# Performance work log

Measured on AMD Instinct MI355X. Metric: run time of the kernel, lower is better.

The kernel has to match this reference:

```python
import jax, jax.numpy as jnp
import numpy as np

D_MODEL = 1024
NUM_HEADS = 16
HEAD_DIM = D_MODEL // NUM_HEADS  # 64
SCALE = HEAD_DIM ** -0.5
BIAS_LEN = 128  # min(max_seq_len=512, 128)
ROPE_BASE = 10000.0
LN_EPS = 1e-5


def setup_inputs() -> dict:
    key = jax.random.key(0)
    ks = jax.random.split(key, 8)
    B, Lq, Lkv = 8, 512, 512
    return {
        "decoder_hidden": jax.random.normal(ks[0], (B, Lq, D_MODEL), jnp.float32),
        "encoder_output": jax.random.normal(ks[1], (B, Lkv, D_MODEL), jnp.float32),
        "Wqkv": jax.random.normal(ks[2], (3 * D_MODEL, D_MODEL), jnp.float32) * 0.02,
        "Wout": jax.random.normal(ks[3], (D_MODEL, D_MODEL), jnp.float32) * 0.02,
        "b_out": jnp.zeros((D_MODEL,), jnp.float32),
        "Wgate": jax.random.normal(ks[4], (D_MODEL, D_MODEL), jnp.float32) * 0.02,
        "b_gate": jnp.zeros((D_MODEL,), jnp.float32),
        "gamma": jnp.ones((D_MODEL,), jnp.float32),
        "beta": jnp.zeros((D_MODEL,), jnp.float32),
    }


def _layernorm(x, gamma, beta):
    mu = jnp.mean(x, axis=-1, keepdims=True)
    var = jnp.mean(jnp.square(x - mu), axis=-1, keepdims=True)
    return (x - mu) * jax.lax.rsqrt(var + LN_EPS) * gamma + beta


def _rope(x, cos, sin):
    # x: [B, H, L, HEAD_DIM]; cos/sin: [L, HEAD_DIM//2]
    half = HEAD_DIM // 2
    c = cos[None, None, :, :]
    s = sin[None, None, :, :]
    x_even, x_odd = x[..., :half], x[..., half:]
    return jnp.concatenate([x_even * c - x_odd * s, x_even * s + x_odd * c], axis=-1)


def _temporal_bias(L_q, L_kv):
    pos = jnp.arange(BIAS_LEN, dtype=jnp.float32)
    dist = jnp.abs(pos[None, :] - pos[:, None])  # [128,128]
    bias = jnp.exp(-dist * 0.1) - dist * 0.05
    if L_q <= BIAS_LEN and L_kv <= BIAS_LEN:
        return bias[:L_q, :L_kv]
    # bilinear interpolation (align_corners=False / half-pixel) fallback
    return jax.image.resize(bias, (L_q, L_kv), method="bilinear")


def reference(decoder_hidden, encoder_output, Wqkv, Wout, b_out, Wgate, b_gate, gamma, beta):
    B, L_q, _ = decoder_hidden.shape
    L_kv = encoder_output.shape[1]
    residual = decoder_hidden

    q_in = _layernorm(decoder_hidden, gamma, beta)
    kv_in = _layernorm(encoder_output, gamma, beta)

    q = q_in @ Wqkv[:D_MODEL].T
    k = kv_in @ Wqkv[D_MODEL:2 * D_MODEL].T
    v = kv_in @ Wqkv[2 * D_MODEL:].T

    q = q.reshape(B, L_q, NUM_HEADS, HEAD_DIM).transpose(0, 2, 1, 3)
    k = k.reshape(B, L_kv, NUM_HEADS, HEAD_DIM).transpose(0, 2, 1, 3)
    v = v.reshape(B, L_kv, NUM_HEADS, HEAD_DIM).transpose(0, 2, 1, 3)

    # rotary embedding over max(L_q, L_kv) positions
    L = max(L_q, L_kv)
    inv_freq = 1.0 / ROPE_BASE ** (jnp.arange(0, HEAD_DIM, 2, dtype=jnp.float32) / HEAD_DIM)
    freqs = jnp.arange(L, dtype=jnp.float32)[:, None] * inv_freq[None, :]  # [L, HEAD_DIM//2]
    cos, sin = jnp.cos(freqs), jnp.sin(freqs)
    q = _rope(q, cos[:L_q], sin[:L_q])
    k = _rope(k, cos[:L_kv], sin[:L_kv])

    scores = jnp.einsum("bhqd,bhkd->bhqk", q, k) * SCALE
    scores = scores + _temporal_bias(L_q, L_kv)[None, None, :, :]

    attn = jax.nn.softmax(scores, axis=-1)
    attended = jnp.einsum("bhqk,bhkd->bhqd", attn, v)
    attended = attended.transpose(0, 2, 1, 3).reshape(B, L_q, D_MODEL)
    attended = attended @ Wout.T + b_out

    gate = jax.nn.sigmoid(attended @ Wgate.T + b_gate)
    output = gate * attended + (1.0 - gate) * residual
    return output
```

## Files before the change

kernel.cpp:

```cpp
#include <hip/hip_runtime.h>
#include <hip/hip_bf16.h>

#define D_MODEL 1024
#define NHEADS 16
#define HDIM 64
#define BATCH 8
#define SEQ 512
#define NROWS 4096
#define SCALE 0.125f
#define LN_EPS 1e-5f

typedef __attribute__((ext_vector_type(8))) short bf16x8;
typedef __attribute__((ext_vector_type(4))) float f32x4;
typedef __attribute__((ext_vector_type(8))) unsigned short u16x8;

static __device__ __forceinline__ float bf2f(unsigned short u) {
    return __uint_as_float(((unsigned int)u) << 16);
}
static __device__ __forceinline__ unsigned short f2bf(float f) {
    unsigned int x = __float_as_uint(f);
    unsigned int r = (x + 0x7fffu + ((x >> 16) & 1u)) >> 16;
    return (unsigned short)r;
}

#define GLOAD16(gp, lp)                                                        \
    __builtin_amdgcn_global_load_lds(                                          \
        (const __attribute__((address_space(1))) void*)(gp),                   \
        (__attribute__((address_space(3))) void*)(lp), 16, 0, 0)

static __device__ __forceinline__ float bias128(int a, int b) {
    float d = fabsf((float)(a - b));
    return expf(-d * 0.1f) - d * 0.05f;
}

__global__ void prep_kernel(const float* __restrict__ dec, const float* __restrict__ enc,
                            const float* __restrict__ gamma, const float* __restrict__ beta,
                            const float* __restrict__ Wqkv,
                            unsigned short* __restrict__ q_ln, unsigned short* __restrict__ kv_ln,
                            float* __restrict__ bias, unsigned short* __restrict__ Wqkv_bf) {
    int blk = blockIdx.x;
    int t = threadIdx.x;
    if (blk >= 9216) {
        int idx = (blk - 9216) * 256 + t;
        float4 v = ((const float4*)Wqkv)[idx];
        ushort4 u;
        u.x = f2bf(v.x); u.y = f2bf(v.y); u.z = f2bf(v.z); u.w = f2bf(v.w);
        ((ushort4*)Wqkv_bf)[idx] = u;
        return;
    }
    if (blk >= 8192) {
        int idx = (blk - 8192) * 256 + t;
        int qi = idx >> 9, kj = idx & 511;
        float fq = (qi + 0.5f) * 0.25f - 0.5f;
        float fk = (kj + 0.5f) * 0.25f - 0.5f;
        int iq = (int)floorf(fq); float tq = fq - (float)iq;
        int ik = (int)floorf(fk); float tk = fk - (float)ik;
        int iq0 = min(max(iq, 0), 127), iq1 = min(max(iq + 1, 0), 127);
        int ik0 = min(max(ik, 0), 127), ik1 = min(max(ik + 1, 0), 127);
        float v = (1.f - tq) * ((1.f - tk) * bias128(iq0, ik0) + tk * bias128(iq0, ik1))
                +        tq  * ((1.f - tk) * bias128(iq1, ik0) + tk * bias128(iq1, ik1));
        bias[idx] = v;
        return;
    }
    int row = blk;
    const float* src = (row < NROWS) ? dec + (size_t)row * D_MODEL
                                     : enc + (size_t)(row - NROWS) * D_MODEL;
    unsigned short* dst = (row < NROWS) ? q_ln + (size_t)row * D_MODEL
                                        : kv_ln + (size_t)(row - NROWS) * D_MODEL;
    float4 x = ((const float4*)src)[t];
    float s  = x.x + x.y + x.z + x.w;
    float ss = x.x * x.x + x.y * x.y + x.z * x.z + x.w * x.w;
    #pragma unroll
    for (int off = 32; off > 0; off >>= 1) {
        s  += __shfl_down(s, off);
        ss += __shfl_down(ss, off);
    }
    __shared__ float red_s[4], red_ss[4];
    int wid = t >> 6, lane = t & 63;
    if (lane == 0) { red_s[wid] = s; red_ss[wid] = ss; }
    __syncthreads();
    if (t == 0) {
        float S = red_s[0] + red_s[1] + red_s[2] + red_s[3];
        float SS = red_ss[0] + red_ss[1] + red_ss[2] + red_ss[3];
        red_s[0] = S; red_ss[0] = SS;
    }
    __syncthreads();
    float mu  = red_s[0] * (1.0f / 1024.0f);
    float var = red_ss[0] * (1.0f / 1024.0f) - mu * mu;
    float rstd = rsqrtf(var + LN_EPS);
    float4 g = ((const float4*)gamma)[t];
    float4 bb = ((const float4*)beta)[t];
    ushort4 u;
    u.x = f2bf((x.x - mu) * rstd * g.x + bb.x);
    u.y = f2bf((x.y - mu) * rstd * g.y + bb.y);
    u.z = f2bf((x.z - mu) * rstd * g.z + bb.z);
    u.w = f2bf((x.w - mu) * rstd * g.w + bb.w);
    ((ushort4*)dst)[t] = u;
}

__global__ void convert_og(const float* __restrict__ Wout, const float* __restrict__ Wgate,
                           unsigned short* __restrict__ Wout_bf, unsigned short* __restrict__ Wgate_bf) {
    int idx = blockIdx.x * 256 + threadIdx.x;
    const float* src; unsigned short* dst; int off;
    if (idx < 262144) { src = (const float*)Wout; dst = Wout_bf; off = idx; }
    else              { src = (const float*)Wgate; dst = Wgate_bf; off = idx - 262144; }
    float4 v = ((const float4*)src)[off];
    ushort4 u;
    u.x = f2bf(v.x); u.y = f2bf(v.y); u.z = f2bf(v.z); u.w = f2bf(v.w);
    ((ushort4*)dst)[off] = u;
}

#define CSTR 136

union alignas(16) GemmSmem {
    struct { unsigned short A[128 * 64]; unsigned short B[128 * 64]; } ab;
    unsigned short C[128 * CSTR];
};

struct alignas(16) Smem64 {
    unsigned short A[64 * 64];
    unsigned short B[128 * 64];
};

#define MF(a, b, d) __builtin_amdgcn_mfma_f32_16x16x32_bf16((a), (b), (d), 0, 0, 0)

#define GEMM_KH(kh)                                                            \
    {                                                                          \
        const unsigned short* Arow_ = &As[(wr * 64 + c) * 64 + pofs##kh];      \
        const unsigned short* Brow_ = &Bs[(wc * 64 + c) * 64 + pofs##kh];      \
        bf16x8 f0 = *(const bf16x8*)(Arow_);                                   \
        bf16x8 f1 = *(const bf16x8*)(Arow_ + 1024);                            \
        bf16x8 f2 = *(const bf16x8*)(Arow_ + 2048);                            \
        bf16x8 f3 = *(const bf16x8*)(Arow_ + 3072);                            \
        bf16x8 g0 = *(const bf16x8*)(Brow_);                                   \
        bf16x8 g1 = *(const bf16x8*)(Brow_ + 1024);                            \
        bf16x8 g2 = *(const bf16x8*)(Brow_ + 2048);                            \
        bf16x8 g3 = *(const bf16x8*)(Brow_ + 3072);                            \
        a00 = MF(f0, g0, a00); a01 = MF(f0, g1, a01); a02 = MF(f0, g2, a02); a03 = MF(f0, g3, a03); \
        a10 = MF(f1, g0, a10); a11 = MF(f1, g1, a11); a12 = MF(f1, g2, a12); a13 = MF(f1, g3, a13); \
        a20 = MF(f2, g0, a20); a21 = MF(f2, g1, a21); a22 = MF(f2, g2, a22); a23 = MF(f2, g3, a23); \
        a30 = MF(f3, g0, a30); a31 = MF(f3, g1, a31); a32 = MF(f3, g2, a32); a33 = MF(f3, g3, a33); \
    }

#define GEMM_MAIN_LOOP(Aptr, Bptr)                                             \
    __shared__ GemmSmem smem;                                                  \
    unsigned short* As = smem.ab.A;                                            \
    unsigned short* Bs = smem.ab.B;                                            \
    int tid = threadIdx.x;                                                     \
    int wave = tid >> 6, lane = tid & 63, quad = lane >> 4, c = lane & 15;     \
    int wr = wave >> 1, wc = wave & 1;                                         \
    int x7 = c & 7;                                                            \
    int pofs0 = (quad ^ x7) * 8;                                               \
    int pofs1 = ((4 + quad) ^ x7) * 8;                                         \
    int grow = lane >> 3;                                                      \
    int cg = ((lane & 7) ^ grow) * 8;                                          \
    const unsigned short* Ag = (Aptr) + (size_t)(rt * 128 + wave * 32 + grow) * 1024 + cg; \
    const unsigned short* Bg = (Bptr) + (size_t)(ct * 128 + wave * 32 + grow) * 1024 + cg; \
    unsigned short* AsW = As + wave * 2048;                                    \
    unsigned short* BsW = Bs + wave * 2048;                                    \
    f32x4 a00 = (f32x4)0.f, a01 = (f32x4)0.f, a02 = (f32x4)0.f, a03 = (f32x4)0.f; \
    f32x4 a10 = (f32x4)0.f, a11 = (f32x4)0.f, a12 = (f32x4)0.f, a13 = (f32x4)0.f; \
    f32x4 a20 = (f32x4)0.f, a21 = (f32x4)0.f, a22 = (f32x4)0.f, a23 = (f32x4)0.f; \
    f32x4 a30 = (f32x4)0.f, a31 = (f32x4)0.f, a32 = (f32x4)0.f, a33 = (f32x4)0.f; \
    for (int kt = 0; kt < 16; ++kt) {                                          \
        int k0 = kt * 64;                                                      \
        __syncthreads();                                                       \
        GLOAD16(Ag + k0,         AsW);                                         \
        GLOAD16(Ag + 8192 + k0,  AsW + 512);                                   \
        GLOAD16(Ag + 16384 + k0, AsW + 1024);                                  \
        GLOAD16(Ag + 24576 + k0, AsW + 1536);                                  \
        GLOAD16(Bg + k0,         BsW);                                         \
        GLOAD16(Bg + 8192 + k0,  BsW + 512);                                   \
        GLOAD16(Bg + 16384 + k0, BsW + 1024);                                  \
        GLOAD16(Bg + 24576 + k0, BsW + 1536);                                  \
        __syncthreads();                                                       \
        GEMM_KH(0)                                                             \
        GEMM_KH(1)                                                             \
    }

#define GEMM_KH2(kh)                                                           \
    {                                                                          \
        const unsigned short* Arow_ = &As2[(wr * 32 + c) * 64 + pofs##kh];     \
        const unsigned short* Brow_ = &Bs2[(wc * 64 + c) * 64 + pofs##kh];     \
        bf16x8 f0 = *(const bf16x8*)(Arow_);                                   \
        bf16x8 f1 = *(const bf16x8*)(Arow_ + 1024);                            \
        bf16x8 g0 = *(const bf16x8*)(Brow_);                                   \
        bf16x8 g1 = *(const bf16x8*)(Brow_ + 1024);                            \
        bf16x8 g2 = *(const bf16x8*)(Brow_ + 2048);                            \
        bf16x8 g3 = *(const bf16x8*)(Brow_ + 3072);                            \
        c00 = MF(f0, g0, c00); c01 = MF(f0, g1, c01); c02 = MF(f0, g2, c02); c03 = MF(f0, g3, c03); \
        c10 = MF(f1, g0, c10); c11 = MF(f1, g1, c11); c12 = MF(f1, g2, c12); c13 = MF(f1, g3, c13); \
    }

#define GEMM_LOOP_64(Aptr, Bptr)                                               \
    __shared__ Smem64 smem2;                                                   \
    unsigned short* As2 = smem2.A;                                             \
    unsigned short* Bs2 = smem2.B;                                             \
    int tid = threadIdx.x;                                                     \
    int wave = tid >> 6, lane = tid & 63, quad = lane >> 4, c = lane & 15;     \
    int wr = wave >> 1, wc = wave & 1;                                         \
    int x7 = c & 7;                                                            \
    int pofs0 = (quad ^ x7) * 8;                                               \
    int pofs1 = ((4 + quad) ^ x7) * 8;                                         \
    int grow = lane >> 3;                                                      \
    int cg = ((lane & 7) ^ grow) * 8;                                          \
    const unsigned short* Ag = (Aptr) + (size_t)(rt * 64 + wave * 16 + grow) * 1024 + cg;  \
    const unsigned short* Bg = (Bptr) + (size_t)(ct * 128 + wave * 32 + grow) * 1024 + cg; \
    unsigned short* AsW = As2 + wave * 1024;                                   \
    unsigned short* BsW = Bs2 + wave * 2048;                                   \
    f32x4 c00 = (f32x4)0.f, c01 = (f32x4)0.f, c02 = (f32x4)0.f, c03 = (f32x4)0.f; \
    f32x4 c10 = (f32x4)0.f, c11 = (f32x4)0.f, c12 = (f32x4)0.f, c13 = (f32x4)0.f; \
    for (int kt = 0; kt < 16; ++kt) {                                          \
        int k0 = kt * 64;                                                      \
        __syncthreads();                                                       \
        GLOAD16(Ag + k0,         AsW);                                         \
        GLOAD16(Ag + 8192 + k0,  AsW + 512);                                   \
        GLOAD16(Bg + k0,         BsW);                                         \
        GLOAD16(Bg + 8192 + k0,  BsW + 512);                                   \
        GLOAD16(Bg + 16384 + k0, BsW + 1024);                                  \
        GLOAD16(Bg + 24576 + k0, BsW + 1536);                                  \
        __syncthreads();                                                       \
        GEMM_KH2(0)                                                            \
        GEMM_KH2(1)                                                            \
    }

#define ROPE_REG(i, reg, A0, A1, A2, A3)                                       \
    {                                                                          \
        int mloc = wr * 64 + (i) * 16 + quad * 4 + (reg);                      \
        int crow = mloc * CSTR + wc * 64;                                      \
        float fl = (float)((rt * 128 + mloc) & 511);                           \
        float aa0 = fl * inv0, aa1 = fl * inv1;                                \
        float c0 = cosf(aa0), s0 = sinf(aa0);                                  \
        float c1 = cosf(aa1), s1 = sinf(aa1);                                  \
        float e0 = A0[(reg)], o0 = A2[(reg)];                                  \
        float e1 = A1[(reg)], o1 = A3[(reg)];                                  \
        smem.C[crow + c]      = f2bf(e0 * c0 - o0 * s0);                       \
        smem.C[crow + 32 + c] = f2bf(e0 * s0 + o0 * c0);                       \
        smem.C[crow + 16 + c] = f2bf(e1 * c1 - o1 * s1);                       \
        smem.C[crow + 48 + c] = f2bf(e1 * s1 + o1 * c1);                       \
    }
#define ROPE_ROW(i, A0, A1, A2, A3)                                            \
    ROPE_REG(i, 0, A0, A1, A2, A3) ROPE_REG(i, 1, A0, A1, A2, A3)              \
    ROPE_REG(i, 2, A0, A1, A2, A3) ROPE_REG(i, 3, A0, A1, A2, A3)

#define VSEC_REG(i, reg, A0, A1, A2, A3)                                       \
    {                                                                          \
        int crow = (wr * 64 + (i) * 16 + quad * 4 + (reg)) * CSTR + wc * 64;   \
        smem.C[crow + c]      = f2bf(A0[(reg)]);                               \
        smem.C[crow + 16 + c] = f2bf(A1[(reg)]);                               \
        smem.C[crow + 32 + c] = f2bf(A2[(reg)]);                               \
        smem.C[crow + 48 + c] = f2bf(A3[(reg)]);                               \
    }
#define VSEC_ROW(i, A0, A1, A2, A3)                                            \
    VSEC_REG(i, 0, A0, A1, A2, A3) VSEC_REG(i, 1, A0, A1, A2, A3)              \
    VSEC_REG(i, 2, A0, A1, A2, A3) VSEC_REG(i, 3, A0, A1, A2, A3)

__global__ __launch_bounds__(256, 1)
void qkv_gemm_mfma(const unsigned short* __restrict__ q_ln,
                   const unsigned short* __restrict__ kv_ln,
                   const unsigned short* __restrict__ Wb,
                   unsigned short* __restrict__ qo,
                   unsigned short* __restrict__ ko,
                   unsigned short* __restrict__ vo) {
    int bid = blockIdx.x;
    int st = bid >> 5, in = bid & 31;
    int stc = st % 3, str = st / 3;
    int ct = stc * 8 + (in & 7);
    int rt = str * 4 + (in >> 3);
    int n0 = ct * 128;
    int section = n0 >> 10;
    const unsigned short* A = (section == 0) ? q_ln : kv_ln;

    GEMM_MAIN_LOOP(A, Wb)

    __syncthreads();
    if (section == 2) {
        VSEC_ROW(0, a00, a01, a02, a03)
        VSEC_ROW(1, a10, a11, a12, a13)
        VSEC_ROW(2, a20, a21, a22, a23)
        VSEC_ROW(3, a30, a31, a32, a33)
    } else {
        float inv0 = expf(-0.2878231366f * (float)c);
        float inv1 = expf(-0.2878231366f * (float)(16 + c));
        ROPE_ROW(0, a00, a01, a02, a03)
        ROPE_ROW(1, a10, a11, a12, a13)
        ROPE_ROW(2, a20, a21, a22, a23)
        ROPE_ROW(3, a30, a31, a32, a33)
    }
    __syncthreads();

    unsigned short* outp = (section == 0) ? qo : (section == 1) ? ko : vo;
    int rr = tid >> 1, ch = tid & 1;
    int mm = rt * 128 + rr;
    int bb = mm >> 9, ll = mm & 511;
    int h = ((n0 & 1023) >> 6) + ch;
    unsigned short* orow = outp + (((size_t)bb * NHEADS + h) * SEQ + ll) * HDIM;
    const unsigned short* csrc = &smem.C[rr * CSTR + ch * 64];
    #pragma unroll
    for (int kc = 0; kc < 8; ++kc)
        *(u16x8*)(orow + kc * 8) = *(const u16x8*)(csrc + kc * 8);
}

#define O1_REG(mb, reg, n, Acc)                                                \
    t_bf[(size_t)((mb) + (reg)) * 1024 + (n)] = f2bf(Acc[(reg)] + bo);
#define O1_TILE(i, j, Acc)                                                     \
    {                                                                          \
        int n = ct * 128 + wc * 64 + (j) * 16 + c;                             \
        float bo = b_out[n];                                                   \
        int mb = rt * 64 + wr * 32 + (i) * 16 + quad * 4;                      \
        O1_REG(mb, 0, n, Acc) O1_REG(mb, 1, n, Acc)                            \
        O1_REG(mb, 2, n, Acc) O1_REG(mb, 3, n, Acc)                            \
    }

__global__ __launch_bounds__(256, 1)
void out_gemm1_mfma(const unsigned short* __restrict__ att,
                    const unsigned short* __restrict__ Wob,
                    const float* __restrict__ b_out,
                    unsigned short* __restrict__ t_bf) {
    int ct = blockIdx.x, rt = blockIdx.y;

    GEMM_LOOP_64(att, Wob)

    O1_TILE(0, 0, c00) O1_TILE(0, 1, c01) O1_TILE(0, 2, c02) O1_TILE(0, 3, c03)
    O1_TILE(1, 0, c10) O1_TILE(1, 1, c11) O1_TILE(1, 2, c12) O1_TILE(1, 3, c13)
}

#define O2_REG(mb, reg, n, Acc)                                                \
    {                                                                          \
        float gz = Acc[(reg)] + bg;                                            \
        float g = 1.0f / (1.0f + expf(-gz));                                   \
        size_t idx = (size_t)((mb) + (reg)) * 1024 + (n);                      \
        float tv = bf2f(t_bf[idx]);                                            \
        float rv = residual[idx];                                              \
        out[idx] = g * tv + (1.0f - g) * rv;                                   \
    }
#define O2_TILE(i, j, Acc)                                                     \
    {                                                                          \
        int n = ct * 128 + wc * 64 + (j) * 16 + c;                             \
        float bg = b_gate[n];                                                  \
        int mb = rt * 64 + wr * 32 + (i) * 16 + quad * 4;                      \
        O2_REG(mb, 0, n, Acc) O2_REG(mb, 1, n, Acc)                            \
        O2_REG(mb, 2, n, Acc) O2_REG(mb, 3, n, Acc)                            \
    }

__global__ __launch_bounds__(256, 1)
void out_gemm2_mfma(const unsigned short* __restrict__ t_bf,
                    const unsigned short* __restrict__ Wgb,
                    const float* __restrict__ b_gate,
                    const float* __restrict__ residual,
                    float* __restrict__ out) {
    int ct = blockIdx.x, rt = blockIdx.y;

    GEMM_LOOP_64(t_bf, Wgb)

    O2_TILE(0, 0, c00) O2_TILE(0, 1, c01) O2_TILE(0, 2, c02) O2_TILE(0, 3, c03)
    O2_TILE(1, 0, c10) O2_TILE(1, 1, c11) O2_TILE(1, 2, c12) O2_TILE(1, 3, c13)
}

#define KSTR 72

__global__ __launch_bounds__(512)
void attn_kernel(const unsigned short* __restrict__ q,
                 const unsigned short* __restrict__ k,
                 const unsigned short* __restrict__ v,
                 const float* __restrict__ bias,
                 unsigned short* __restrict__ attended) {
    int qt = blockIdx.x, h = blockIdx.y, b = blockIdx.z;
    __shared__ unsigned short Ks[64 * KSTR];
    __shared__ unsigned short Vt[64 * KSTR];
    __shared__ unsigned short Ps[128 * KSTR];
    __shared__ float lf[128];

    int tid = threadIdx.x;
    int wave = tid >> 6, lane = tid & 63;
    int quad = lane >> 4, c = lane & 15;
    int wb = wave * 16;
    size_t headbase = (((size_t)b * NHEADS + h) * SEQ) * HDIM;
    int q0 = qt * 128;

    const unsigned short* qrow = q + headbase + (size_t)(q0 + wb + c) * HDIM;
    bf16x8 aq0 = *(const bf16x8*)(qrow + quad * 8);
    bf16x8 aq1 = *(const bf16x8*)(qrow + 32 + quad * 8);

    int sr = tid >> 3, sc0 = (tid & 7) * 8;

    f32x4 oacc[4];
    #pragma unroll
    for (int t = 0; t < 4; ++t) oacc[t] = (f32x4)0.f;
    float lrow[4];
    #pragma unroll
    for (int r = 0; r < 4; ++r) lrow[r] = 0.f;

    for (int kt = 0; kt < 8; ++kt) {
        int kv0 = kt * 64;
        __syncthreads();
        {
            const unsigned short* krow = k + headbase + (size_t)(kv0 + sr) * HDIM + sc0;
            const unsigned short* vrow = v + headbase + (size_t)(kv0 + sr) * HDIM + sc0;
            u16x8 ka = *(const u16x8*)(krow);
            u16x8 va = *(const u16x8*)(vrow);
            *(u16x8*)&Ks[sr * KSTR + sc0] = ka;
            #pragma unroll
            for (int j = 0; j < 8; ++j) Vt[(sc0 + j) * KSTR + sr] = va[j];
        }
        __syncthreads();

        f32x4 sacc[4];
        #pragma unroll
        for (int nt = 0; nt < 4; ++nt) {
            const unsigned short* kbase = &Ks[(nt * 16 + c) * KSTR];
            bf16x8 b0 = *(const bf16x8*)(kbase + quad * 8);
            bf16x8 b1 = *(const bf16x8*)(kbase + 32 + quad * 8);
            f32x4 a = (f32x4)0.f;
            a = __builtin_amdgcn_mfma_f32_16x16x32_bf16(aq0, b0, a, 0, 0, 0);
            a = __builtin_amdgcn_mfma_f32_16x16x32_bf16(aq1, b1, a, 0, 0, 0);
            sacc[nt] = a;
        }

        const float* bbase = bias + (size_t)(q0 + wb + quad * 4) * 512 + kv0 + c;
        float tsum[4];
        #pragma unroll
        for (int r = 0; r < 4; ++r) tsum[r] = 0.f;
        #pragma unroll
        for (int nt = 0; nt < 4; ++nt)
            #pragma unroll
            for (int r = 0; r < 4; ++r) {
                float p = __expf(sacc[nt][r] * SCALE + bbase[(size_t)r * 512 + nt * 16]);
                tsum[r] += p;
                Ps[(wb + quad * 4 + r) * KSTR + nt * 16 + c] = f2bf(p);
            }
        #pragma unroll
        for (int r = 0; r < 4; ++r) {
            float t = tsum[r];
            t += __shfl_xor(t, 1);
            t += __shfl_xor(t, 2);
            t += __shfl_xor(t, 4);
            t += __shfl_xor(t, 8);
            lrow[r] += t;
        }

        bf16x8 pb0 = *(const bf16x8*)&Ps[(wb + c) * KSTR + quad * 8];
        bf16x8 pb1 = *(const bf16x8*)&Ps[(wb + c) * KSTR + 32 + quad * 8];
        #pragma unroll
        for (int t = 0; t < 4; ++t) {
            const unsigned short* vbase = &Vt[(t * 16 + c) * KSTR];
            bf16x8 a0 = *(const bf16x8*)(vbase + quad * 8);
            bf16x8 a1 = *(const bf16x8*)(vbase + 32 + quad * 8);
            oacc[t] = __builtin_amdgcn_mfma_f32_16x16x32_bf16(a0, pb0, oacc[t], 0, 0, 0);
            oacc[t] = __builtin_amdgcn_mfma_f32_16x16x32_bf16(a1, pb1, oacc[t], 0, 0, 0);
        }
    }

    if (c == 0) {
        f32x4 lv;
        lv[0] = lrow[0]; lv[1] = lrow[1]; lv[2] = lrow[2]; lv[3] = lrow[3];
        *(f32x4*)&lf[wb + quad * 4] = lv;
    }
    float invl = 1.0f / lf[wb + c];
    unsigned short* drow = attended + ((size_t)b * SEQ + (q0 + wb + c)) * D_MODEL + h * HDIM;
    #pragma unroll
    for (int t = 0; t < 4; ++t) {
        ushort4 o;
        o.x = f2bf(oacc[t][0] * invl);
        o.y = f2bf(oacc[t][1] * invl);
        o.z = f2bf(oacc[t][2] * invl);
        o.w = f2bf(oacc[t][3] * invl);
        *(ushort4*)(drow + t * 16 + quad * 4) = o;
    }
}

extern "C" void kernel_launch(void* const* d_in, const int* in_sizes, int n_in,
                              void* d_out, int out_size, void* d_ws, size_t ws_size,
                              hipStream_t stream) {
    const float* dec    = (const float*)d_in[0];
    const float* enc    = (const float*)d_in[1];
    const float* Wqkv   = (const float*)d_in[2];
    const float* Wout   = (const float*)d_in[3];
    const float* b_out  = (const float*)d_in[4];
    const float* Wgate  = (const float*)d_in[5];
    const float* b_gate = (const float*)d_in[6];
    const float* gamma  = (const float*)d_in[7];
    const float* beta   = (const float*)d_in[8];
    float* out = (float*)d_out;

    char* ws = (char*)d_ws;
    const size_t MB = 1024 * 1024;
    unsigned short* q_ln    = (unsigned short*)(ws + 0 * MB);
    unsigned short* kv_ln   = (unsigned short*)(ws + 8 * MB);
    unsigned short* qb      = (unsigned short*)(ws + 16 * MB);
    unsigned short* kb      = (unsigned short*)(ws + 24 * MB);
    unsigned short* vb      = (unsigned short*)(ws + 32 * MB);
    unsigned short* Wqkv_bf = (unsigned short*)(ws + 40 * MB);
    float*          bias    = (float*)(ws + 46 * MB);
    unsigned short* att     = (unsigned short*)(ws + 0 * MB);
    unsigned short* t_bf    = (unsigned short*)(ws + 24 * MB);
    unsigned short* Wout_bf = (unsigned short*)(ws + 32 * MB);
    unsigned short* Wgate_bf= (unsigned short*)(ws + 34 * MB);

    prep_kernel<<<12288, 256, 0, stream>>>(dec, enc, gamma, beta, Wqkv,
                                           q_ln, kv_ln, bias, Wqkv_bf);
    qkv_gemm_mfma<<<768, 256, 0, stream>>>(q_ln, kv_ln, Wqkv_bf, qb, kb, vb);
    attn_kernel<<<dim3(4, 16, 8), 512, 0, stream>>>(qb, kb, vb, bias, att);
    convert_og<<<2048, 256, 0, stream>>>(Wout, Wgate, Wout_bf, Wgate_bf);
    out_gemm1_mfma<<<dim3(8, 64), 256, 0, stream>>>(att, Wout_bf, b_out, t_bf);
    out_gemm2_mfma<<<dim3(8, 64), 256, 0, stream>>>(t_bf, Wgate_bf, b_gate, dec, out);
}
```

Baseline: 244.3 us.

## Deepen K tile in output GEMMs and fold Wout/Wgate conversion into prep

The two output-projection GEMMs now stage 128-wide K slices instead of 64, halving the loop trip count and the number of barrier pairs per K sweep. Shared memory per block grows to 48KB. The Wout/Wgate bf16 conversion is merged into the prep kernel as extra blocks when the workspace is large enough, removing one kernel launch. The swizzle pattern changes to a 16-way XOR to fit the wider rows.

```diff
diff --git a/kernel.cpp b/kernel.cpp
--- a/kernel.cpp
+++ b/kernel.cpp
@@ -36,10 +36,23 @@
 __global__ void prep_kernel(const float* __restrict__ dec, const float* __restrict__ enc,
                             const float* __restrict__ gamma, const float* __restrict__ beta,
                             const float* __restrict__ Wqkv,
+                            const float* __restrict__ Wout, const float* __restrict__ Wgate,
                             unsigned short* __restrict__ q_ln, unsigned short* __restrict__ kv_ln,
-                            float* __restrict__ bias, unsigned short* __restrict__ Wqkv_bf) {
+                            float* __restrict__ bias, unsigned short* __restrict__ Wqkv_bf,
+                            unsigned short* __restrict__ Wout_bf, unsigned short* __restrict__ Wgate_bf) {
     int blk = blockIdx.x;
     int t = threadIdx.x;
+    if (blk >= 12288) {
+        int idx = (blk - 12288) * 256 + t;
+        const float* src; unsigned short* dst; int off;
+        if (idx < 262144) { src = Wout; dst = Wout_bf; off = idx; }
+        else              { src = Wgate; dst = Wgate_bf; off = idx - 262144; }
+        float4 v = ((const float4*)src)[off];
+        ushort4 u;
+        u.x = f2bf(v.x); u.y = f2bf(v.y); u.z = f2bf(v.z); u.w = f2bf(v.w);
+        ((ushort4*)dst)[off] = u;
+        return;
+    }
     if (blk >= 9216) {
         int idx = (blk - 9216) * 256 + t;
         float4 v = ((const float4*)Wqkv)[idx];
@@ -117,9 +130,9 @@
     unsigned short C[128 * CSTR];
 };
 
-struct alignas(16) Smem64 {
-    unsigned short A[64 * 64];
-    unsigned short B[128 * 64];
+struct alignas(16) Smem64B {
+    unsigned short A[64 * 128];
+    unsigned short B[128 * 128];
 };
 
 #define MF(a, b, d) __builtin_amdgcn_mfma_f32_16x16x32_bf16((a), (b), (d), 0, 0, 0)
@@ -178,50 +191,67 @@
         GEMM_KH(1)                                                             \
     }
 
-#define GEMM_KH2(kh)                                                           \
-    {                                                                          \
-        const unsigned short* Arow_ = &As2[(wr * 32 + c) * 64 + pofs##kh];     \
-        const unsigned short* Brow_ = &Bs2[(wc * 64 + c) * 64 + pofs##kh];     \
+#define GEMM_KH2B(kh)                                                          \
+    {                                                                          \
+        int pofs = (((kh) * 4 + quad) ^ c) * 8;                                \
+        const unsigned short* Arow_ = &As2[(wr * 32 + c) * 128 + pofs];        \
+        const unsigned short* Brow_ = &Bs2[(wc * 64 + c) * 128 + pofs];        \
         bf16x8 f0 = *(const bf16x8*)(Arow_);                                   \
-        bf16x8 f1 = *(const bf16x8*)(Arow_ + 1024);                            \
+        bf16x8 f1 = *(const bf16x8*)(Arow_ + 2048);                            \
         bf16x8 g0 = *(const bf16x8*)(Brow_);                                   \
-        bf16x8 g1 = *(const bf16x8*)(Brow_ + 1024);                            \
-        bf16x8 g2 = *(const bf16x8*)(Brow_ + 2048);                            \
-        bf16x8 g3 = *(const bf16x8*)(Brow_ + 3072);                            \
+        bf16x8 g1 = *(const bf16x8*)(Brow_ + 2048);                            \
+        bf16x8 g2 = *(const bf16x8*)(Brow_ + 4096);                            \
+        bf16x8 g3 = *(const bf16x8*)(Brow_ + 6144);                            \
         c00 = MF(f0, g0, c00); c01 = MF(f0, g1, c01); c02 = MF(f0, g2, c02); c03 = MF(f0, g3, c03); \
         c10 = MF(f1, g0, c10); c11 = MF(f1, g1, c11); c12 = MF(f1, g2, c12); c13 = MF(f1, g3, c13); \
     }
 
-#define GEMM_LOOP_64(Aptr, Bptr)                                               \
-    __shared__ Smem64 smem2;                                                   \
+#define GEMM_LOOP_64B(Aptr, Bptr)                                              \
+    __shared__ Smem64B smem2;                                                  \
     unsigned short* As2 = smem2.A;                                             \
     unsigned short* Bs2 = smem2.B;                                             \
     int tid = threadIdx.x;                                                     \
     int wave = tid >> 6, lane = tid & 63, quad = lane >> 4, c = lane & 15;     \
     int wr = wave >> 1, wc = wave & 1;                                         \
-    int x7 = c & 7;                                                            \
-    int pofs0 = (quad ^ x7) * 8;                                               \
-    int pofs1 = ((4 + quad) ^ x7) * 8;                                         \
-    int grow = lane >> 3;                                                      \
-    int cg = ((lane & 7) ^ grow) * 8;                                          \
-    const unsigned short* Ag = (Aptr) + (size_t)(rt * 64 + wave * 16 + grow) * 1024 + cg;  \
-    const unsigned short* Bg = (Bptr) + (size_t)(ct * 128 + wave * 32 + grow) * 1024 + cg; \
-    unsigned short* AsW = As2 + wave * 1024;                                   \
-    unsigned short* BsW = Bs2 + wave * 2048;                                   \
+    int l4 = lane >> 4, l15 = lane & 15;                                       \
+    const unsigned short* Abase = (Aptr) + (size_t)(rt * 64) * 1024;           \
+    const unsigned short* Bbase = (Bptr) + (size_t)(ct * 128) * 1024;          \
+    int aoff0 = (wave * 16 +  0 + l4) * 1024 + ((l15 ^ ( 0 + l4)) * 8);        \
+    int aoff1 = (wave * 16 +  4 + l4) * 1024 + ((l15 ^ ( 4 + l4)) * 8);        \
+    int aoff2 = (wave * 16 +  8 + l4) * 1024 + ((l15 ^ ( 8 + l4)) * 8);        \
+    int aoff3 = (wave * 16 + 12 + l4) * 1024 + ((l15 ^ (12 + l4)) * 8);        \
+    int boff0 = (wave * 32 +  0 + l4) * 1024 + ((l15 ^ (( 0 + l4) & 15)) * 8); \
+    int boff1 = (wave * 32 +  4 + l4) * 1024 + ((l15 ^ (( 4 + l4) & 15)) * 8); \
+    int boff2 = (wave * 32 +  8 + l4) * 1024 + ((l15 ^ (( 8 + l4) & 15)) * 8); \
+    int boff3 = (wave * 32 + 12 + l4) * 1024 + ((l15 ^ ((12 + l4) & 15)) * 8); \
+    int boff4 = (wave * 32 + 16 + l4) * 1024 + ((l15 ^ ((16 + l4) & 15)) * 8); \
+    int boff5 = (wave * 32 + 20 + l4) * 1024 + ((l15 ^ ((20 + l4) & 15)) * 8); \
+    int boff6 = (wave * 32 + 24 + l4) * 1024 + ((l15 ^ ((24 + l4) & 15)) * 8); \
+    int boff7 = (wave * 32 + 28 + l4) * 1024 + ((l15 ^ ((28 + l4) & 15)) * 8); \
+    unsigned short* AsW = As2 + wave * 2048;                                   \
+    unsigned short* BsW = Bs2 + wave * 4096;                                   \
     f32x4 c00 = (f32x4)0.f, c01 = (f32x4)0.f, c02 = (f32x4)0.f, c03 = (f32x4)0.f; \
     f32x4 c10 = (f32x4)0.f, c11 = (f32x4)0.f, c12 = (f32x4)0.f, c13 = (f32x4)0.f; \
-    for (int kt = 0; kt < 16; ++kt) {                                          \
-        int k0 = kt * 64;                                                      \
+    for (int kt = 0; kt < 8; ++kt) {                                           \
+        int k0 = kt * 128;                                                     \
         __syncthreads();                                                       \
-        GLOAD16(Ag + k0,         AsW);                                         \
-        GLOAD16(Ag + 8192 + k0,  AsW + 512);                                   \
-        GLOAD16(Bg + k0,         BsW);                                         \
-        GLOAD16(Bg + 8192 + k0,  BsW + 512);                                   \
-        GLOAD16(Bg + 16384 + k0, BsW + 1024);                                  \
-        GLOAD16(Bg + 24576 + k0, BsW + 1536);                                  \
+        GLOAD16(Abase + aoff0 + k0, AsW);                                      \
+        GLOAD16(Abase + aoff1 + k0, AsW + 512);                                \
+        GLOAD16(Abase + aoff2 + k0, AsW + 1024);                               \
+        GLOAD16(Abase + aoff3 + k0, AsW + 1536);                               \
+        GLOAD16(Bbase + boff0 + k0, BsW);                                      \
+        GLOAD16(Bbase + boff1 + k0, BsW + 512);                                \
+        GLOAD16(Bbase + boff2 + k0, BsW + 1024);                               \
+        GLOAD16(Bbase + boff3 + k0, BsW + 1536);                               \
+        GLOAD16(Bbase + boff4 + k0, BsW + 2048);                               \
+        GLOAD16(Bbase + boff5 + k0, BsW + 2560);                               \
+        GLOAD16(Bbase + boff6 + k0, BsW + 3072);                               \
+        GLOAD16(Bbase + boff7 + k0, BsW + 3584);                               \
         __syncthreads();                                                       \
-        GEMM_KH2(0)                                                            \
-        GEMM_KH2(1)                                                            \
+        GEMM_KH2B(0)                                                           \
+        GEMM_KH2B(1)                                                           \
+        GEMM_KH2B(2)                                                           \
+        GEMM_KH2B(3)                                                           \
     }
 
 #define ROPE_REG(i, reg, A0, A1, A2, A3)                                       \
@@ -319,7 +349,7 @@
                     unsigned short* __restrict__ t_bf) {
     int ct = blockIdx.x, rt = blockIdx.y;
 
-    GEMM_LOOP_64(att, Wob)
+    GEMM_LOOP_64B(att, Wob)
 
     O1_TILE(0, 0, c00) O1_TILE(0, 1, c01) O1_TILE(0, 2, c02) O1_TILE(0, 3, c03)
     O1_TILE(1, 0, c10) O1_TILE(1, 1, c11) O1_TILE(1, 2, c12) O1_TILE(1, 3, c13)
@@ -351,7 +381,7 @@
                     float* __restrict__ out) {
     int ct = blockIdx.x, rt = blockIdx.y;
 
-    GEMM_LOOP_64(t_bf, Wgb)
+    GEMM_LOOP_64B(t_bf, Wgb)
 
     O2_TILE(0, 0, c00) O2_TILE(0, 1, c01) O2_TILE(0, 2, c02) O2_TILE(0, 3, c03)
     O2_TILE(1, 0, c10) O2_TILE(1, 1, c11) O2_TILE(1, 2, c12) O2_TILE(1, 3, c13)
@@ -494,14 +524,18 @@
     float*          bias    = (float*)(ws + 46 * MB);
     unsigned short* att     = (unsigned short*)(ws + 0 * MB);
     unsigned short* t_bf    = (unsigned short*)(ws + 24 * MB);
-    unsigned short* Wout_bf = (unsigned short*)(ws + 32 * MB);
-    unsigned short* Wgate_bf= (unsigned short*)(ws + 34 * MB);
-
-    prep_kernel<<<12288, 256, 0, stream>>>(dec, enc, gamma, beta, Wqkv,
-                                           q_ln, kv_ln, bias, Wqkv_bf);
+
+    bool hoist = (ws_size >= 51 * MB);
+    unsigned short* Wout_bf  = (unsigned short*)(ws + (hoist ? 47 * MB : 32 * MB));
+    unsigned short* Wgate_bf = (unsigned short*)(ws + (hoist ? 49 * MB : 34 * MB));
+
+    prep_kernel<<<hoist ? 14336 : 12288, 256, 0, stream>>>(
+        dec, enc, gamma, beta, Wqkv, Wout, Wgate,
+        q_ln, kv_ln, bias, Wqkv_bf, Wout_bf, Wgate_bf);
     qkv_gemm_mfma<<<768, 256, 0, stream>>>(q_ln, kv_ln, Wqkv_bf, qb, kb, vb);
     attn_kernel<<<dim3(4, 16, 8), 512, 0, stream>>>(qb, kb, vb, bias, att);
-    convert_og<<<2048, 256, 0, stream>>>(Wout, Wgate, Wout_bf, Wgate_bf);
+    if (!hoist)
+        convert_og<<<2048, 256, 0, stream>>>(Wout, Wgate, Wout_bf, Wgate_bf);
     out_gemm1_mfma<<<dim3(8, 64), 256, 0, stream>>>(att, Wout_bf, b_out, t_bf);
     out_gemm2_mfma<<<dim3(8, 64), 256, 0, stream>>>(t_bf, Wgate_bf, b_gate, dec, out);
 }
```

Result: faster. 237.5 us (-2.8%).
